# Optimization experiments

Hardware: AMD Instinct MI355X
Metric: run time of the kernel (lower is better)

Reference implementation:

```python
import jax, jax.numpy as jnp
import numpy as np
from jax import lax
from jax.scipy.special import logsumexp

B, L, H, T = 64, 512, 768, 16


def setup_inputs() -> dict:
    key = jax.random.key(0)
    ks = jax.random.split(key, 6)
    return {
        "hidden_state": jax.random.normal(ks[0], (B, L, H), dtype=jnp.float32),
        "attention_mask": jnp.ones((B, L), dtype=jnp.int32),
        "labels": jax.random.randint(ks[1], (B, L), 0, T),
        "classifier_w": jax.random.normal(ks[2], (T, H), dtype=jnp.float32) * 0.02,
        "classifier_b": jnp.zeros((T,), dtype=jnp.float32),
        "start_trans": jax.random.normal(ks[3], (T,), dtype=jnp.float32) * 0.1,
        "end_trans": jax.random.normal(ks[4], (T,), dtype=jnp.float32) * 0.1,
        "trans": jax.random.normal(ks[5], (T,), dtype=jnp.float32)[:, None] * 0.0
                 + jax.random.normal(ks[5], (T, T), dtype=jnp.float32) * 0.1,
    }


def _crf_numerator(emissions, labels, mask, start_trans, end_trans, trans):
    # emissions [B,L,T], labels [B,L], mask [B,L] float
    em = jnp.take_along_axis(emissions, labels[..., None], axis=-1)[..., 0]  # [B,L]
    tr = trans[labels[:, :-1], labels[:, 1:]]                                # [B,L-1]
    score = start_trans[labels[:, 0]] + em[:, 0]
    score = score + jnp.sum(mask[:, 1:] * (tr + em[:, 1:]), axis=1)
    seq_ends = jnp.sum(mask, axis=1).astype(jnp.int32) - 1                   # [B]
    last_tags = jnp.take_along_axis(labels, seq_ends[:, None], axis=1)[:, 0]
    return score + end_trans[last_tags]


def _crf_denominator(emissions, mask, start_trans, end_trans, trans):
    # forward algorithm with masking; scan over time
    init = start_trans[None, :] + emissions[:, 0]  # [B,T]

    def step(score, xs):
        m, em = xs  # m [B], em [B,T]
        nxt = logsumexp(score[:, :, None] + trans[None] + em[:, None, :], axis=1)
        score = jnp.where(m[:, None] > 0, nxt, score)
        return score, None

    xs = (jnp.swapaxes(mask[:, 1:], 0, 1), jnp.swapaxes(emissions[:, 1:], 0, 1))
    final, _ = lax.scan(step, init, xs)
    return logsumexp(final + end_trans[None, :], axis=1)  # [B]


def _viterbi_single(emissions, start_trans, end_trans, trans):
    # emissions [L,T]; decode without mask (as in the torch code: self.crf.decode(logits))
    score0 = start_trans + emissions[0]

    def step(score, em):
        nxt = score[:, None] + trans + em[None, :]  # [T,T]
        return jnp.max(nxt, axis=0), jnp.argmax(nxt, axis=0)

    final, history = lax.scan(step, score0, emissions[1:])  # history [L-1,T]
    last = jnp.argmax(final + end_trans)

    def back(tag, hist):
        prev = hist[tag]
        return prev, prev

    _, tags_rev = lax.scan(back, last, history, reverse=True)
    return jnp.concatenate([tags_rev, last[None]])  # [L]


def reference(hidden_state, attention_mask, labels, classifier_w, classifier_b,
              start_trans, end_trans, trans):
    # dropout is identity at inference/reference time
    logits = jnp.einsum("blh,th->blt", hidden_state, classifier_w) + classifier_b  # [B,L,T]
    maskf = attention_mask.astype(logits.dtype)
    numer = _crf_numerator(logits, labels, maskf, start_trans, end_trans, trans)
    denom = _crf_denominator(logits, maskf, start_trans, end_trans, trans)
    llh = numer - denom
    loss = -jnp.mean(llh)  # reduction='mean' over batch
    tags = jax.vmap(_viterbi_single, in_axes=(0, None, None, None))(
        logits, start_trans, end_trans, trans)  # [B,L] int
    return loss, tags.astype(jnp.float32)
```

## Files before the change

### kernel.cpp

```cpp
#include <hip/hip_runtime.h>
#include <cstdint>

#define Bn 64
#define Ln 512
#define Hn 768
#define Tn 16
#define Cn 8
#define Sn 64
#define Kn 4
#define Kc 192
#define Mrows (Bn*Ln)
#define LOG16 2.7725887222397812f

__global__ __launch_bounds__(256) void k_gemm_part(
    const float* __restrict__ hs, const float* __restrict__ W,
    float* __restrict__ partial, float* __restrict__ lossws) {
  int bx = blockIdx.x;
  if (bx == 0 && threadIdx.x == 0) {
    lossws[0] = 0.f;
    ((int*)lossws)[1] = 0;
  }
  int rt = bx >> 2, s = bx & 3;
  int tid = threadIdx.x;
  int r0 = rt * 128, kb = s * Kc;
  int row = (tid & 63) + ((tid >> 7) << 6);
  int t0 = ((tid >> 6) & 1) * 8;
  __shared__ float alds[128 * 36];
  __shared__ float wlds[16 * 192];
  float acc[8] = {0.f};
#pragma unroll
  for (int idx = tid; idx < 768; idx += 256) {
    int t = idx / 48, jj = idx - t * 48;
    *(float4*)&wlds[t * 192 + jj * 4] = *(const float4*)(W + (size_t)t * Hn + kb + jj * 4);
  }
#pragma unroll 1
  for (int cc = 0; cc < 6; ++cc) {
    int k0 = kb + cc * 32;
#pragma unroll
    for (int it = 0; it < 4; ++it) {
      int f = it * 256 + tid;
      int r = f >> 3, j = f & 7;
      float4 v = *(const float4*)(hs + (size_t)(r0 + r) * Hn + k0 + j * 4);
      *(float4*)&alds[r * 36 + j * 4] = v;
    }
    __syncthreads();
#pragma unroll
    for (int j = 0; j < 8; ++j) {
      float4 a = *(const float4*)&alds[row * 36 + j * 4];
#pragma unroll
      for (int tt = 0; tt < 8; ++tt) {
        float4 wv = *(const float4*)&wlds[(t0 + tt) * 192 + cc * 32 + j * 4];
        acc[tt] = fmaf(a.x, wv.x, fmaf(a.y, wv.y, fmaf(a.z, wv.z, fmaf(a.w, wv.w, acc[tt]))));
      }
    }
    __syncthreads();
  }
  float* dst = partial + ((size_t)s * Mrows + (r0 + row)) * Tn + t0;
  *(float4*)(dst + 0) = make_float4(acc[0], acc[1], acc[2], acc[3]);
  *(float4*)(dst + 4) = make_float4(acc[4], acc[5], acc[6], acc[7]);
}

__global__ __launch_bounds__(256) void k_em_scan(
    const float* __restrict__ partial, const float* __restrict__ bias,
    const int* __restrict__ mask, const float* __restrict__ trans,
    float* __restrict__ em, float* __restrict__ qmat,
    float* __restrict__ qv, uint8_t* __restrict__ hist) {
  int half = blockIdx.x >> 9, bc = blockIdx.x & 511;
  int b = bc >> 3, c = bc & 7;
  int tid = threadIdx.x, i = tid >> 4, tp = tid & 15;
  int l0 = c * Sn;
  __shared__ float ems[Sn * Tn];
  __shared__ int msk[Sn];
  __shared__ float pbuf[256];
  __shared__ uint8_t hl[Tn * Sn * Tn];
#pragma unroll
  for (int g = 0; g < 4; ++g) {
    int rl = (tid >> 4) + g * 16, t = tid & 15;
    int grow = bc * Sn + rl;
    float sum = bias[t];
#pragma unroll
    for (int s = 0; s < Kn; ++s) sum += partial[((size_t)s * Mrows + grow) * Tn + t];
    float mx = sum;
    mx = fmaxf(mx, __shfl_xor(mx, 1));
    mx = fmaxf(mx, __shfl_xor(mx, 2));
    mx = fmaxf(mx, __shfl_xor(mx, 4));
    mx = fmaxf(mx, __shfl_xor(mx, 8));
    float ev = sum - (mx + LOG16);
    ems[rl * Tn + t] = ev;
    if (half == 0) em[(size_t)grow * Tn + t] = ev;
  }
  if (tid < Sn) msk[tid] = mask[b * Ln + l0 + tid];
  __syncthreads();
  int lstart = (c == 0) ? 1 : l0;
  int gb = i << 4;
  if (half == 0) {
    float etr[Tn];
#pragma unroll
    for (int t = 0; t < Tn; ++t) etr[t] = __expf(trans[t * Tn + tp]);
    float p = (tp == i) ? 1.f : 0.f;
    float logs = 0.f;
    for (int l = lstart; l < l0 + Sn; ++l) {
      pbuf[tid] = p;
      __builtin_amdgcn_sched_barrier(0);
      float4 q0 = *(const float4*)&pbuf[gb + 0];
      float4 q1 = *(const float4*)&pbuf[gb + 4];
      float4 q2 = *(const float4*)&pbuf[gb + 8];
      float4 q3 = *(const float4*)&pbuf[gb + 12];
      float cs = __expf(ems[(l - l0) * Tn + tp]);
      float dot = 0.f;
      dot = fmaf(q0.x, etr[0],  dot); dot = fmaf(q0.y, etr[1],  dot);
      dot = fmaf(q0.z, etr[2],  dot); dot = fmaf(q0.w, etr[3],  dot);
      dot = fmaf(q1.x, etr[4],  dot); dot = fmaf(q1.y, etr[5],  dot);
      dot = fmaf(q1.z, etr[6],  dot); dot = fmaf(q1.w, etr[7],  dot);
      dot = fmaf(q2.x, etr[8],  dot); dot = fmaf(q2.y, etr[9],  dot);
      dot = fmaf(q2.z, etr[10], dot); dot = fmaf(q2.w, etr[11], dot);
      dot = fmaf(q3.x, etr[12], dot); dot = fmaf(q3.y, etr[13], dot);
      dot = fmaf(q3.z, etr[14], dot); dot = fmaf(q3.w, etr[15], dot);
      float pn = dot * cs;
      p = msk[l - l0] ? pn : p;
      if ((l & 15) == 15) {
        float m = p;
        m = fmaxf(m, __shfl_xor(m, 1));
        m = fmaxf(m, __shfl_xor(m, 2));
        m = fmaxf(m, __shfl_xor(m, 4));
        m = fmaxf(m, __shfl_xor(m, 8));
        p /= m;
        logs += __logf(m);
      }
    }
    qmat[(((size_t)b * Cn + c) * Tn + i) * Tn + tp] = __logf(p) + logs;
  } else {
    float tcol[Tn];
#pragma unroll
    for (int t = 0; t < Tn; ++t) tcol[t] = trans[t * Tn + tp];
    float v = (tp == i) ? 0.f : -1e30f;
    for (int l = lstart; l < l0 + Sn; ++l) {
      pbuf[tid] = v;
      __builtin_amdgcn_sched_barrier(0);
      float4 q0 = *(const float4*)&pbuf[gb + 0];
      float4 q1 = *(const float4*)&pbuf[gb + 4];
      float4 q2 = *(const float4*)&pbuf[gb + 8];
      float4 q3 = *(const float4*)&pbuf[gb + 12];
      float best = -3.0e38f; int arg = 0;
#define VSTEP(val, t) { float cand = (val) + tcol[t]; bool g = cand > best; \
                        arg = g ? (t) : arg; best = g ? cand : best; }
      VSTEP(q0.x, 0)  VSTEP(q0.y, 1)  VSTEP(q0.z, 2)  VSTEP(q0.w, 3)
      VSTEP(q1.x, 4)  VSTEP(q1.y, 5)  VSTEP(q1.z, 6)  VSTEP(q1.w, 7)
      VSTEP(q2.x, 8)  VSTEP(q2.y, 9)  VSTEP(q2.z, 10) VSTEP(q2.w, 11)
      VSTEP(q3.x, 12) VSTEP(q3.y, 13) VSTEP(q3.z, 14) VSTEP(q3.w, 15)
#undef VSTEP
      v = best + ems[(l - l0) * Tn + tp];
      hl[(i * Sn + (l - l0)) * Tn + tp] = (uint8_t)arg;
    }
    qv[(((size_t)b * Cn + c) * Tn + i) * Tn + tp] = v;
    __syncthreads();
    const uint4* s4 = (const uint4*)hl;
    uint4* d4 = (uint4*)(hist + (size_t)bc * (Tn * Sn * Tn));
    for (int k = tid; k < (Tn * Sn * Tn) / 16; k += 256) d4[k] = s4[k];
  }
}

__global__ __launch_bounds__(512) void k_tail(
    const float* __restrict__ qv, const float* __restrict__ em,
    const float* __restrict__ start, const float* __restrict__ endt,
    const uint8_t* __restrict__ hist, const int* __restrict__ labels,
    const int* __restrict__ mask, const float* __restrict__ trans,
    const float* __restrict__ qmat, float* __restrict__ lossws,
    float* __restrict__ loss_out, float* __restrict__ tags) {
  int bid = blockIdx.x, tid = threadIdx.x;
  if (bid >= Bn) {
    int b = bid - Bn;
    {
      int l = tid;
      int y = labels[b * Ln + l];
      int m = mask[b * Ln + l];
      float s;
      if (l == 0) s = start[y] + em[((size_t)b * Ln) * Tn + y];
      else s = m ? (trans[labels[b * Ln + l - 1] * Tn + y] + em[((size_t)b * Ln + l) * Tn + y]) : 0.f;
      int msum = m;
      for (int off = 32; off; off >>= 1) {
        s += __shfl_down(s, off);
        msum += __shfl_down(msum, off);
      }
      __shared__ float sw[8]; __shared__ int mw[8];
      __shared__ float snum;
      int wid = tid >> 6, ln = tid & 63;
      if (ln == 0) { sw[wid] = s; mw[wid] = msum; }
      __syncthreads();
      if (tid == 0) {
        float st = 0.f; int mt = 0;
        for (int wv = 0; wv < 8; ++wv) { st += sw[wv]; mt += mw[wv]; }
        snum = st + endt[labels[b * Ln + mt - 1]];
      }
      __syncthreads();
      if (tid < Tn) {
        int k = tid;
        float p = start[k] + em[((size_t)b * Ln) * Tn + k];
        for (int c = 0; c < Cn; ++c) {
          float vals[Tn]; float mx = -3.0e38f;
#pragma unroll
          for (int i2 = 0; i2 < Tn; ++i2) {
            float cand = __shfl(p, i2, 16) + qmat[(((size_t)b * Cn + c) * Tn + i2) * Tn + k];
            vals[i2] = cand;
            mx = fmaxf(mx, cand);
          }
          float sm = 0.f;
#pragma unroll
          for (int i2 = 0; i2 < Tn; ++i2) sm += __expf(vals[i2] - mx);
          p = mx + __logf(sm);
        }
        float x = p + endt[k];
        float mx = x;
        mx = fmaxf(mx, __shfl_xor(mx, 1));
        mx = fmaxf(mx, __shfl_xor(mx, 2));
        mx = fmaxf(mx, __shfl_xor(mx, 4));
        mx = fmaxf(mx, __shfl_xor(mx, 8));
        float e = __expf(x - mx);
        e += __shfl_xor(e, 1);
        e += __shfl_xor(e, 2);
        e += __shfl_xor(e, 4);
        e += __shfl_xor(e, 8);
        float denom = mx + __logf(e);
        if (k == 0) {
          atomicAdd(&lossws[0], snum - denom);
          __threadfence();
          int ticket = atomicAdd((int*)lossws + 1, 1);
          if (ticket == Bn - 1) {
            __threadfence();
            float total = atomicAdd(&lossws[0], 0.f);
            loss_out[0] = -total * (1.0f / Bn);
          }
        }
      }
    }
    return;
  }
  int b = bid;
  __shared__ int Bs[Cn][Tn];
  __shared__ int bnd[Cn + 1];
  if (tid < Tn) {
    int k = tid;
    float p = start[k] + em[((size_t)b * Ln) * Tn + k];
    for (int c = 0; c < Cn; ++c) {
      float best = -3.0e38f; int arg = 0;
#pragma unroll
      for (int i2 = 0; i2 < Tn; ++i2) {
        float cand = __shfl(p, i2, 16) + qv[(((size_t)b * Cn + c) * Tn + i2) * Tn + k];
        bool g = cand > best;
        arg = g ? i2 : arg;
        best = g ? cand : best;
      }
      Bs[c][k] = arg;
      p = best;
    }
    float x = p + endt[k]; int idx = k;
#pragma unroll
    for (int d = 1; d < 16; d <<= 1) {
      float xo = __shfl_xor(x, d);
      int io = __shfl_xor(idx, d);
      bool take = (xo > x) || (xo == x && io < idx);
      x = take ? xo : x;
      idx = take ? io : idx;
    }
    if (k == 0) bnd[Cn] = idx;
  }
  __syncthreads();
  if (tid == 0) {
    int t = bnd[Cn];
    for (int c = Cn - 1; c >= 0; --c) { t = Bs[c][t]; bnd[c] = t; }
  }
  __syncthreads();
  int w = tid >> 6, lane = tid & 63;
  int istar = bnd[w];
  int cur = bnd[w + 1];
  int l0 = w * Sn;
  const uint4* hp = (const uint4*)(hist + ((size_t)(b * Cn + w) * Tn + istar) * (Sn * Tn));
  uint4 hh = hp[lane];
  float mytag = (lane == 63) ? (float)cur : 0.f;
  for (int l = l0 + 63; l >= l0 + 1; --l) {
    int sl = l - l0;
    unsigned w0 = __shfl((int)hh.x, sl);
    unsigned w1 = __shfl((int)hh.y, sl);
    unsigned w2 = __shfl((int)hh.z, sl);
    unsigned w3 = __shfl((int)hh.w, sl);
    unsigned word = (cur < 8) ? ((cur < 4) ? w0 : w1) : ((cur < 12) ? w2 : w3);
    cur = (int)((word >> ((cur & 3) * 8)) & 0xff);
    if (lane == sl - 1) mytag = (float)cur;
  }
  tags[(size_t)b * Ln + l0 + lane] = mytag;
}

extern "C" void kernel_launch(void* const* d_in, const int* in_sizes, int n_in,
                              void* d_out, int out_size, void* d_ws, size_t ws_size,
                              hipStream_t stream) {
  const float* hs     = (const float*)d_in[0];
  const int*   mask   = (const int*)d_in[1];
  const int*   labels = (const int*)d_in[2];
  const float* W      = (const float*)d_in[3];
  const float* bias   = (const float*)d_in[4];
  const float* start  = (const float*)d_in[5];
  const float* endt   = (const float*)d_in[6];
  const float* trans  = (const float*)d_in[7];
  float* out = (float*)d_out;

  char* ws = (char*)d_ws;
  float*   em      = (float*)(ws);
  float*   qmat    = (float*)(ws + 2097152);
  float*   qv      = (float*)(ws + 2621440);
  float*   lossws  = (float*)(ws + 3145728);
  float*   partial = (float*)(ws + 3149824);
  uint8_t* hist    = (uint8_t*)(ws + 11538432);

  hipLaunchKernelGGL(k_gemm_part, dim3(1024), dim3(256), 0, stream, hs, W, partial, lossws);
  hipLaunchKernelGGL(k_em_scan,   dim3(1024), dim3(256), 0, stream, partial, bias, mask, trans, em, qmat, qv, hist);
  hipLaunchKernelGGL(k_tail,      dim3(128),  dim3(512), 0, stream, qv, em, start, endt, hist, labels, mask, trans, qmat, lossws, out, out + 1);
}
```

Baseline: 209.1 us.

## Fuse CRF tail into scan kernel via per-batch last-block atomic counter

Removes the separate tail kernel. Each of the 16 scan blocks for a batch row bumps a per-batch counter after a threadfence, and the last one to arrive computes the numerator, the forward log-partition, the loss accumulation and the Viterbi backtrace for that row. The counters are zeroed in the GEMM kernel. This saves a launch and lets tail work overlap with scan blocks still running for other rows. The cost is that one 256-thread block now runs both the loss and decode paths serially, with the backtrace split into two passes per wave.

```diff
diff --git a/kernel.cpp b/kernel.cpp
--- a/kernel.cpp
+++ b/kernel.cpp
@@ -16,19 +16,18 @@
     const float* __restrict__ hs, const float* __restrict__ W,
     float* __restrict__ partial, float* __restrict__ lossws) {
   int bx = blockIdx.x;
-  if (bx == 0 && threadIdx.x == 0) {
-    lossws[0] = 0.f;
-    ((int*)lossws)[1] = 0;
+  int tid = threadIdx.x;
+  if (bx == 0) {
+    if (tid == 0) { lossws[0] = 0.f; ((int*)lossws)[1] = 0; }
+    if (tid < Bn) ((int*)(lossws + 64))[tid] = 0;
   }
   int rt = bx >> 2, s = bx & 3;
-  int tid = threadIdx.x;
   int r0 = rt * 128, kb = s * Kc;
   int row = (tid & 63) + ((tid >> 7) << 6);
   int t0 = ((tid >> 6) & 1) * 8;
   __shared__ float alds[128 * 36];
   __shared__ float wlds[16 * 192];
   float acc[8] = {0.f};
-#pragma unroll
   for (int idx = tid; idx < 768; idx += 256) {
     int t = idx / 48, jj = idx - t * 48;
     *(float4*)&wlds[t * 192 + jj * 4] = *(const float4*)(W + (size_t)t * Hn + kb + jj * 4);
@@ -63,8 +62,12 @@
 __global__ __launch_bounds__(256) void k_em_scan(
     const float* __restrict__ partial, const float* __restrict__ bias,
     const int* __restrict__ mask, const float* __restrict__ trans,
+    const int* __restrict__ labels, const float* __restrict__ start,
+    const float* __restrict__ endt,
     float* __restrict__ em, float* __restrict__ qmat,
-    float* __restrict__ qv, uint8_t* __restrict__ hist) {
+    float* __restrict__ qv, uint8_t* __restrict__ hist,
+    float* __restrict__ lossws, float* __restrict__ loss_out,
+    float* __restrict__ tags) {
   int half = blockIdx.x >> 9, bc = blockIdx.x & 511;
   int b = bc >> 3, c = bc & 7;
   int tid = threadIdx.x, i = tid >> 4, tp = tid & 15;
@@ -73,6 +76,9 @@
   __shared__ int msk[Sn];
   __shared__ float pbuf[256];
   __shared__ uint8_t hl[Tn * Sn * Tn];
+  __shared__ int amwin;
+  __shared__ float sw[4]; __shared__ int mw[4]; __shared__ float snum;
+  __shared__ int Bs[Cn][Tn]; __shared__ int bnd[Cn + 1];
 #pragma unroll
   for (int g = 0; g < 4; ++g) {
     int rl = (tid >> 4) + g * 16, t = tid & 15;
@@ -158,99 +164,90 @@
     uint4* d4 = (uint4*)(hist + (size_t)bc * (Tn * Sn * Tn));
     for (int k = tid; k < (Tn * Sn * Tn) / 16; k += 256) d4[k] = s4[k];
   }
-}
-
-__global__ __launch_bounds__(512) void k_tail(
-    const float* __restrict__ qv, const float* __restrict__ em,
-    const float* __restrict__ start, const float* __restrict__ endt,
-    const uint8_t* __restrict__ hist, const int* __restrict__ labels,
-    const int* __restrict__ mask, const float* __restrict__ trans,
-    const float* __restrict__ qmat, float* __restrict__ lossws,
-    float* __restrict__ loss_out, float* __restrict__ tags) {
-  int bid = blockIdx.x, tid = threadIdx.x;
-  if (bid >= Bn) {
-    int b = bid - Bn;
-    {
-      int l = tid;
+  __threadfence();
+  __syncthreads();
+  if (tid == 0) {
+    int* bdone = (int*)(lossws + 64);
+    amwin = (atomicAdd(&bdone[b], 1) == 15);
+  }
+  __syncthreads();
+  if (!amwin) return;
+  __threadfence();
+  {
+    float s = 0.f; int msum = 0;
+    for (int l = tid; l < Ln; l += 256) {
       int y = labels[b * Ln + l];
       int m = mask[b * Ln + l];
-      float s;
-      if (l == 0) s = start[y] + em[((size_t)b * Ln) * Tn + y];
-      else s = m ? (trans[labels[b * Ln + l - 1] * Tn + y] + em[((size_t)b * Ln + l) * Tn + y]) : 0.f;
-      int msum = m;
-      for (int off = 32; off; off >>= 1) {
-        s += __shfl_down(s, off);
-        msum += __shfl_down(msum, off);
-      }
-      __shared__ float sw[8]; __shared__ int mw[8];
-      __shared__ float snum;
-      int wid = tid >> 6, ln = tid & 63;
-      if (ln == 0) { sw[wid] = s; mw[wid] = msum; }
-      __syncthreads();
-      if (tid == 0) {
-        float st = 0.f; int mt = 0;
-        for (int wv = 0; wv < 8; ++wv) { st += sw[wv]; mt += mw[wv]; }
-        snum = st + endt[labels[b * Ln + mt - 1]];
-      }
-      __syncthreads();
-      if (tid < Tn) {
-        int k = tid;
-        float p = start[k] + em[((size_t)b * Ln) * Tn + k];
-        for (int c = 0; c < Cn; ++c) {
-          float vals[Tn]; float mx = -3.0e38f;
-#pragma unroll
-          for (int i2 = 0; i2 < Tn; ++i2) {
-            float cand = __shfl(p, i2, 16) + qmat[(((size_t)b * Cn + c) * Tn + i2) * Tn + k];
-            vals[i2] = cand;
-            mx = fmaxf(mx, cand);
-          }
-          float sm = 0.f;
-#pragma unroll
-          for (int i2 = 0; i2 < Tn; ++i2) sm += __expf(vals[i2] - mx);
-          p = mx + __logf(sm);
-        }
-        float x = p + endt[k];
-        float mx = x;
-        mx = fmaxf(mx, __shfl_xor(mx, 1));
-        mx = fmaxf(mx, __shfl_xor(mx, 2));
-        mx = fmaxf(mx, __shfl_xor(mx, 4));
-        mx = fmaxf(mx, __shfl_xor(mx, 8));
-        float e = __expf(x - mx);
-        e += __shfl_xor(e, 1);
-        e += __shfl_xor(e, 2);
-        e += __shfl_xor(e, 4);
-        e += __shfl_xor(e, 8);
-        float denom = mx + __logf(e);
-        if (k == 0) {
-          atomicAdd(&lossws[0], snum - denom);
-          __threadfence();
-          int ticket = atomicAdd((int*)lossws + 1, 1);
-          if (ticket == Bn - 1) {
-            __threadfence();
-            float total = atomicAdd(&lossws[0], 0.f);
-            loss_out[0] = -total * (1.0f / Bn);
-          }
-        }
-      }
-    }
-    return;
-  }
-  int b = bid;
-  __shared__ int Bs[Cn][Tn];
-  __shared__ int bnd[Cn + 1];
+      msum += m;
+      if (l == 0) s += start[y] + em[((size_t)b * Ln) * Tn + y];
+      else if (m) s += trans[labels[b * Ln + l - 1] * Tn + y] + em[((size_t)b * Ln + l) * Tn + y];
+    }
+    for (int off = 32; off; off >>= 1) {
+      s += __shfl_down(s, off);
+      msum += __shfl_down(msum, off);
+    }
+    int wid = tid >> 6, ln = tid & 63;
+    if (ln == 0) { sw[wid] = s; mw[wid] = msum; }
+  }
+  __syncthreads();
+  if (tid == 0) {
+    float st = sw[0] + sw[1] + sw[2] + sw[3];
+    int mt = mw[0] + mw[1] + mw[2] + mw[3];
+    snum = st + endt[labels[b * Ln + mt - 1]];
+  }
+  __syncthreads();
   if (tid < Tn) {
     int k = tid;
     float p = start[k] + em[((size_t)b * Ln) * Tn + k];
-    for (int c = 0; c < Cn; ++c) {
+    for (int cc2 = 0; cc2 < Cn; ++cc2) {
+      float vals[Tn]; float mx = -3.0e38f;
+#pragma unroll
+      for (int i2 = 0; i2 < Tn; ++i2) {
+        float cand = __shfl(p, i2, 16) + qmat[(((size_t)b * Cn + cc2) * Tn + i2) * Tn + k];
+        vals[i2] = cand;
+        mx = fmaxf(mx, cand);
+      }
+      float sm = 0.f;
+#pragma unroll
+      for (int i2 = 0; i2 < Tn; ++i2) sm += __expf(vals[i2] - mx);
+      p = mx + __logf(sm);
+    }
+    float x = p + endt[k];
+    float mx = x;
+    mx = fmaxf(mx, __shfl_xor(mx, 1));
+    mx = fmaxf(mx, __shfl_xor(mx, 2));
+    mx = fmaxf(mx, __shfl_xor(mx, 4));
+    mx = fmaxf(mx, __shfl_xor(mx, 8));
+    float e = __expf(x - mx);
+    e += __shfl_xor(e, 1);
+    e += __shfl_xor(e, 2);
+    e += __shfl_xor(e, 4);
+    e += __shfl_xor(e, 8);
+    float denom = mx + __logf(e);
+    if (k == 0) {
+      atomicAdd(&lossws[0], snum - denom);
+      __threadfence();
+      int ticket = atomicAdd((int*)lossws + 1, 1);
+      if (ticket == Bn - 1) {
+        __threadfence();
+        float total = atomicAdd(&lossws[0], 0.f);
+        loss_out[0] = -total * (1.0f / Bn);
+      }
+    }
+  }
+  if (tid < Tn) {
+    int k = tid;
+    float p = start[k] + em[((size_t)b * Ln) * Tn + k];
+    for (int cc2 = 0; cc2 < Cn; ++cc2) {
       float best = -3.0e38f; int arg = 0;
 #pragma unroll
       for (int i2 = 0; i2 < Tn; ++i2) {
-        float cand = __shfl(p, i2, 16) + qv[(((size_t)b * Cn + c) * Tn + i2) * Tn + k];
+        float cand = __shfl(p, i2, 16) + qv[(((size_t)b * Cn + cc2) * Tn + i2) * Tn + k];
         bool g = cand > best;
         arg = g ? i2 : arg;
         best = g ? cand : best;
       }
-      Bs[c][k] = arg;
+      Bs[cc2][k] = arg;
       p = best;
     }
     float x = p + endt[k]; int idx = k;
@@ -267,27 +264,31 @@
   __syncthreads();
   if (tid == 0) {
     int t = bnd[Cn];
-    for (int c = Cn - 1; c >= 0; --c) { t = Bs[c][t]; bnd[c] = t; }
-  }
-  __syncthreads();
-  int w = tid >> 6, lane = tid & 63;
-  int istar = bnd[w];
-  int cur = bnd[w + 1];
-  int l0 = w * Sn;
-  const uint4* hp = (const uint4*)(hist + ((size_t)(b * Cn + w) * Tn + istar) * (Sn * Tn));
-  uint4 hh = hp[lane];
-  float mytag = (lane == 63) ? (float)cur : 0.f;
-  for (int l = l0 + 63; l >= l0 + 1; --l) {
-    int sl = l - l0;
-    unsigned w0 = __shfl((int)hh.x, sl);
-    unsigned w1 = __shfl((int)hh.y, sl);
-    unsigned w2 = __shfl((int)hh.z, sl);
-    unsigned w3 = __shfl((int)hh.w, sl);
-    unsigned word = (cur < 8) ? ((cur < 4) ? w0 : w1) : ((cur < 12) ? w2 : w3);
-    cur = (int)((word >> ((cur & 3) * 8)) & 0xff);
-    if (lane == sl - 1) mytag = (float)cur;
-  }
-  tags[(size_t)b * Ln + l0 + lane] = mytag;
+    for (int cc2 = Cn - 1; cc2 >= 0; --cc2) { t = Bs[cc2][t]; bnd[cc2] = t; }
+  }
+  __syncthreads();
+  int w0id = tid >> 6, lane = tid & 63;
+#pragma unroll
+  for (int hh2 = 0; hh2 < 2; ++hh2) {
+    int w = w0id + hh2 * 4;
+    int istar = bnd[w];
+    int cur = bnd[w + 1];
+    int lc0 = w * Sn;
+    const uint4* hp = (const uint4*)(hist + ((size_t)(b * Cn + w) * Tn + istar) * (Sn * Tn));
+    uint4 hh = hp[lane];
+    float mytag = (lane == 63) ? (float)cur : 0.f;
+    for (int l = lc0 + 63; l >= lc0 + 1; --l) {
+      int sl = l - lc0;
+      unsigned w0v = __shfl((int)hh.x, sl);
+      unsigned w1v = __shfl((int)hh.y, sl);
+      unsigned w2v = __shfl((int)hh.z, sl);
+      unsigned w3v = __shfl((int)hh.w, sl);
+      unsigned word = (cur < 8) ? ((cur < 4) ? w0v : w1v) : ((cur < 12) ? w2v : w3v);
+      cur = (int)((word >> ((cur & 3) * 8)) & 0xff);
+      if (lane == sl - 1) mytag = (float)cur;
+    }
+    tags[(size_t)b * Ln + lc0 + lane] = mytag;
+  }
 }
 
 extern "C" void kernel_launch(void* const* d_in, const int* in_sizes, int n_in,
@@ -312,6 +313,7 @@
   uint8_t* hist    = (uint8_t*)(ws + 11538432);
 
   hipLaunchKernelGGL(k_gemm_part, dim3(1024), dim3(256), 0, stream, hs, W, partial, lossws);
-  hipLaunchKernelGGL(k_em_scan,   dim3(1024), dim3(256), 0, stream, partial, bias, mask, trans, em, qmat, qv, hist);
-  hipLaunchKernelGGL(k_tail,      dim3(128),  dim3(512), 0, stream, qv, em, start, endt, hist, labels, mask, trans, qmat, lossws, out, out + 1);
+  hipLaunchKernelGGL(k_em_scan,   dim3(1024), dim3(256), 0, stream,
+                     partial, bias, mask, trans, labels, start, endt,
+                     em, qmat, qv, hist, lossws, out, out + 1);
 }
```

Result: slower. 307.1 us (+46.9%).

## Drop split-K GEMM partials; fuse bias and log-normalize into GEMM with register prefetch

Applied to the files above, without the earlier changes.

The GEMM no longer splits the K dimension across four blocks. Each block now computes the full 768-long dot product for 128 rows, holding the whole W slice in LDS and prefetching the next hidden-state chunk into registers. Bias add and max-based normalization happen in the GEMM epilogue, which writes em directly. This removes the partial buffer's global write and read and its reduction in the scan kernel. The cost is only 256 blocks on a 256-CU device, so parallelism and latency hiding drop, and the larger LDS footprint (about 70KB) limits occupancy.

```diff
diff --git a/kernel.cpp b/kernel.cpp
--- a/kernel.cpp
+++ b/kernel.cpp
@@ -7,63 +7,85 @@
 #define Tn 16
 #define Cn 8
 #define Sn 64
-#define Kn 4
 #define Kc 192
 #define Mrows (Bn*Ln)
 #define LOG16 2.7725887222397812f
 
-__global__ __launch_bounds__(256) void k_gemm_part(
+__global__ __launch_bounds__(256) void k_gemm_em(
     const float* __restrict__ hs, const float* __restrict__ W,
-    float* __restrict__ partial, float* __restrict__ lossws) {
+    const float* __restrict__ bias, float* __restrict__ em,
+    float* __restrict__ lossws) {
   int bx = blockIdx.x;
-  if (bx == 0 && threadIdx.x == 0) {
+  int tid = threadIdx.x;
+  if (bx == 0 && tid == 0) {
     lossws[0] = 0.f;
     ((int*)lossws)[1] = 0;
   }
-  int rt = bx >> 2, s = bx & 3;
-  int tid = threadIdx.x;
-  int r0 = rt * 128, kb = s * Kc;
+  int r0 = bx * 128;
   int row = (tid & 63) + ((tid >> 7) << 6);
   int t0 = ((tid >> 6) & 1) * 8;
   __shared__ float alds[128 * 36];
-  __shared__ float wlds[16 * 192];
-  float acc[8] = {0.f};
-#pragma unroll
-  for (int idx = tid; idx < 768; idx += 256) {
-    int t = idx / 48, jj = idx - t * 48;
-    *(float4*)&wlds[t * 192 + jj * 4] = *(const float4*)(W + (size_t)t * Hn + kb + jj * 4);
-  }
+  __shared__ float wlds[16 * 768];
+  __shared__ float sums[128 * 17];
+  float acc[4][8] = {{0.f}};
+  for (int idx = tid; idx < 3072; idx += 256) {
+    int t = idx / 192, jj = idx - t * 192;
+    *(float4*)&wlds[t * 768 + jj * 4] = *(const float4*)(W + (size_t)t * Hn + jj * 4);
+  }
+  int sr[4], sj[4];
+#pragma unroll
+  for (int it = 0; it < 4; ++it) { int f = it * 256 + tid; sr[it] = f >> 3; sj[it] = f & 7; }
+  float4 pv[4];
+#pragma unroll
+  for (int it = 0; it < 4; ++it)
+    pv[it] = *(const float4*)(hs + (size_t)(r0 + sr[it]) * Hn + sj[it] * 4);
+#pragma unroll
+  for (int s = 0; s < 4; ++s) {
 #pragma unroll 1
-  for (int cc = 0; cc < 6; ++cc) {
-    int k0 = kb + cc * 32;
-#pragma unroll
-    for (int it = 0; it < 4; ++it) {
-      int f = it * 256 + tid;
-      int r = f >> 3, j = f & 7;
-      float4 v = *(const float4*)(hs + (size_t)(r0 + r) * Hn + k0 + j * 4);
-      *(float4*)&alds[r * 36 + j * 4] = v;
-    }
-    __syncthreads();
-#pragma unroll
-    for (int j = 0; j < 8; ++j) {
-      float4 a = *(const float4*)&alds[row * 36 + j * 4];
-#pragma unroll
-      for (int tt = 0; tt < 8; ++tt) {
-        float4 wv = *(const float4*)&wlds[(t0 + tt) * 192 + cc * 32 + j * 4];
-        acc[tt] = fmaf(a.x, wv.x, fmaf(a.y, wv.y, fmaf(a.z, wv.z, fmaf(a.w, wv.w, acc[tt]))));
-      }
-    }
-    __syncthreads();
-  }
-  float* dst = partial + ((size_t)s * Mrows + (r0 + row)) * Tn + t0;
-  *(float4*)(dst + 0) = make_float4(acc[0], acc[1], acc[2], acc[3]);
-  *(float4*)(dst + 4) = make_float4(acc[4], acc[5], acc[6], acc[7]);
+    for (int cc = 0; cc < 6; ++cc) {
+      int k0 = s * Kc + cc * 32;
+#pragma unroll
+      for (int it = 0; it < 4; ++it)
+        *(float4*)&alds[sr[it] * 36 + sj[it] * 4] = pv[it];
+      __syncthreads();
+      if (k0 < 736) {
+#pragma unroll
+        for (int it = 0; it < 4; ++it)
+          pv[it] = *(const float4*)(hs + (size_t)(r0 + sr[it]) * Hn + (k0 + 32) + sj[it] * 4);
+      }
+#pragma unroll
+      for (int j = 0; j < 8; ++j) {
+        float4 a = *(const float4*)&alds[row * 36 + j * 4];
+#pragma unroll
+        for (int tt = 0; tt < 8; ++tt) {
+          float4 wv = *(const float4*)&wlds[(t0 + tt) * 768 + k0 + j * 4];
+          acc[s][tt] = fmaf(a.x, wv.x, fmaf(a.y, wv.y, fmaf(a.z, wv.z, fmaf(a.w, wv.w, acc[s][tt]))));
+        }
+      }
+      __syncthreads();
+    }
+  }
+#pragma unroll
+  for (int tt = 0; tt < 8; ++tt) {
+    float sum = bias[t0 + tt];
+    sum += acc[0][tt]; sum += acc[1][tt]; sum += acc[2][tt]; sum += acc[3][tt];
+    sums[row * 17 + t0 + tt] = sum;
+  }
+  __syncthreads();
+  float mx = sums[row * 17 + 0];
+#pragma unroll
+  for (int t = 1; t < 16; ++t) mx = fmaxf(mx, sums[row * 17 + t]);
+  float mlog = mx + LOG16;
+  float* dst = em + (size_t)(r0 + row) * Tn + t0;
+  *(float4*)(dst + 0) = make_float4(sums[row * 17 + t0 + 0] - mlog, sums[row * 17 + t0 + 1] - mlog,
+                                    sums[row * 17 + t0 + 2] - mlog, sums[row * 17 + t0 + 3] - mlog);
+  *(float4*)(dst + 4) = make_float4(sums[row * 17 + t0 + 4] - mlog, sums[row * 17 + t0 + 5] - mlog,
+                                    sums[row * 17 + t0 + 6] - mlog, sums[row * 17 + t0 + 7] - mlog);
 }
 
 __global__ __launch_bounds__(256) void k_em_scan(
-    const float* __restrict__ partial, const float* __restrict__ bias,
-    const int* __restrict__ mask, const float* __restrict__ trans,
-    float* __restrict__ em, float* __restrict__ qmat,
+    const float* __restrict__ em, const int* __restrict__ mask,
+    const float* __restrict__ trans, float* __restrict__ qmat,
     float* __restrict__ qv, uint8_t* __restrict__ hist) {
   int half = blockIdx.x >> 9, bc = blockIdx.x & 511;
   int b = bc >> 3, c = bc & 7;
@@ -73,21 +95,9 @@
   __shared__ int msk[Sn];
   __shared__ float pbuf[256];
   __shared__ uint8_t hl[Tn * Sn * Tn];
-#pragma unroll
-  for (int g = 0; g < 4; ++g) {
-    int rl = (tid >> 4) + g * 16, t = tid & 15;
-    int grow = bc * Sn + rl;
-    float sum = bias[t];
-#pragma unroll
-    for (int s = 0; s < Kn; ++s) sum += partial[((size_t)s * Mrows + grow) * Tn + t];
-    float mx = sum;
-    mx = fmaxf(mx, __shfl_xor(mx, 1));
-    mx = fmaxf(mx, __shfl_xor(mx, 2));
-    mx = fmaxf(mx, __shfl_xor(mx, 4));
-    mx = fmaxf(mx, __shfl_xor(mx, 8));
-    float ev = sum - (mx + LOG16);
-    ems[rl * Tn + t] = ev;
-    if (half == 0) em[(size_t)grow * Tn + t] = ev;
+  {
+    int rl = tid >> 2, q = tid & 3;
+    *(float4*)&ems[rl * Tn + q * 4] = *(const float4*)(em + (size_t)(bc * Sn + rl) * Tn + q * 4);
   }
   if (tid < Sn) msk[tid] = mask[b * Ln + l0 + tid];
   __syncthreads();
@@ -308,10 +318,9 @@
   float*   qmat    = (float*)(ws + 2097152);
   float*   qv      = (float*)(ws + 2621440);
   float*   lossws  = (float*)(ws + 3145728);
-  float*   partial = (float*)(ws + 3149824);
-  uint8_t* hist    = (uint8_t*)(ws + 11538432);
-
-  hipLaunchKernelGGL(k_gemm_part, dim3(1024), dim3(256), 0, stream, hs, W, partial, lossws);
-  hipLaunchKernelGGL(k_em_scan,   dim3(1024), dim3(256), 0, stream, partial, bias, mask, trans, em, qmat, qv, hist);
-  hipLaunchKernelGGL(k_tail,      dim3(128),  dim3(512), 0, stream, qv, em, start, endt, hist, labels, mask, trans, qmat, lossws, out, out + 1);
+  uint8_t* hist    = (uint8_t*)(ws + 3149824);
+
+  hipLaunchKernelGGL(k_gemm_em, dim3(256),  dim3(256), 0, stream, hs, W, bias, em, lossws);
+  hipLaunchKernelGGL(k_em_scan, dim3(1024), dim3(256), 0, stream, em, mask, trans, qmat, qv, hist);
+  hipLaunchKernelGGL(k_tail,    dim3(128),  dim3(512), 0, stream, qv, em, start, endt, hist, labels, mask, trans, qmat, lossws, out, out + 1);
 }
```

Result: slower. 271.0 us (+29.6%).
